# Kernel optimization log

Hardware: AMD Instinct MI355X
Metric: run time of the kernel (lower is better)

Reference implementation:

```python
import jax, jax.numpy as jnp
import numpy as np

B, S, D, H, F, M = 2, 2048, 1024, 16, 4096, 1024
HD = D // H
LR, MOM_DECAY, WD, THRESH = 0.01, 0.9, 0.01, 0.1


def rmsnorm(x, w, eps=1e-8):
    n = jnp.linalg.norm(x, axis=-1, keepdims=True) * (x.shape[-1] ** -0.5)
    return w * x / (n + eps)


def rope_sin_cos(seq_len, dim):
    inv_freq = 1.0 / (10000.0 ** (jnp.arange(0, dim, 2, dtype=jnp.float32) / dim))
    ang = jnp.arange(seq_len, dtype=jnp.float32)[:, None] * inv_freq[None, :]  # [S, dim/2]
    return jnp.sin(ang), jnp.cos(ang)


def apply_rope(x, sin, cos):
    # x: [B,H,S,hd]; sin/cos: [S,hd/2] broadcast. Matches torch source:
    # split even/odd lanes, then CONCATENATE halves (not interleave).
    x1, x2 = x[..., ::2], x[..., 1::2]
    return jnp.concatenate([x1 * cos - x2 * sin, x1 * sin + x2 * cos], axis=-1)


def lmm_mlp(z, w0, b0, w1, b1):
    return jnp.maximum(z @ w0 + b0, 0.0) @ w1 + b1


def setup_inputs() -> dict:
    key = jax.random.key(0)
    k = jax.random.split(key, 20)
    sc = 0.02
    r = lambda i, shape: jax.random.normal(k[i], shape, jnp.float32) * sc
    return {
        'x': jax.random.normal(k[0], (B, S, D), jnp.float32),
        'mask': jnp.tril(jnp.ones((1, 1, S, S), dtype=bool)),
        'wq': r(1, (D, D)), 'wk': r(2, (D, D)), 'wv': r(3, (D, D)), 'wo': r(4, (D, D)),
        'n1': jnp.ones(D, jnp.float32), 'n2': jnp.ones(D, jnp.float32), 'n3': jnp.ones(D, jnp.float32),
        'ffn_w1': r(5, (D, F)), 'ffn_w2': r(6, (D, F)), 'ffn_w3': r(7, (F, D)),
        'pk_w': r(8, (D, M)), 'pk_b': jnp.zeros(M, jnp.float32),
        'pv_w': r(9, (D, M)), 'pv_b': jnp.zeros(M, jnp.float32),
        'pq_w': r(10, (D, M)), 'pq_b': jnp.zeros(M, jnp.float32),
        'l0_w': r(11, (M, M)), 'l0_b': jnp.zeros(M, jnp.float32),
        'l1_w': r(12, (M, M)), 'l1_b': jnp.zeros(M, jnp.float32),
        'm0_w': jnp.zeros((M, M), jnp.float32), 'm0_b': jnp.zeros(M, jnp.float32),
        'm1_w': jnp.zeros((M, M), jnp.float32), 'm1_b': jnp.zeros(M, jnp.float32),
    }


def reference(x, mask, wq, wk, wv, wo, n1, n2, n3, ffn_w1, ffn_w2, ffn_w3,
              pk_w, pk_b, pv_w, pv_b, pq_w, pq_b,
              l0_w, l0_b, l1_w, l1_b, m0_w, m0_b, m1_w, m1_b):
    # ---- attention sublayer (pre-norm, RoPE) ----
    hn = rmsnorm(x, n1)
    q = (hn @ wq).reshape(B, S, H, HD).transpose(0, 2, 1, 3)
    kk = (hn @ wk).reshape(B, S, H, HD).transpose(0, 2, 1, 3)
    v = (hn @ wv).reshape(B, S, H, HD).transpose(0, 2, 1, 3)
    sin, cos = rope_sin_cos(S, HD)
    q = apply_rope(q, sin, cos)
    kk = apply_rope(kk, sin, cos)
    scores = jnp.einsum('bhqd,bhkd->bhqk', q, kk) / np.sqrt(HD).astype(np.float32)
    scores = jnp.where(mask, scores, -jnp.inf)
    attn = jax.nn.softmax(scores, axis=-1)
    o = jnp.einsum('bhqk,bhkd->bhqd', attn, v).transpose(0, 2, 1, 3).reshape(B, S, D)
    h = x + o @ wo

    # ---- neural memory sublayer ----
    hn2 = rmsnorm(h, n2)
    q_lmm = hn2 @ pq_w + pq_b
    retrieved = lmm_mlp(q_lmm, l0_w, l0_b, l1_w, l1_b)  # uses PRE-update params

    # online Titan-style LMM update (torch does this under no_grad, after retrieval)
    kf = jax.lax.stop_gradient((hn2 @ pk_w + pk_b).reshape(B * S, M))
    vf = jax.lax.stop_gradient((hn2 @ pv_w + pv_b).reshape(B * S, M))

    def lmm_loss(params):
        pred = lmm_mlp(kf, *params)
        return jnp.sum(jnp.mean((pred - vf) ** 2, axis=-1))

    params = (l0_w, l0_b, l1_w, l1_b)
    loss_sum, grads = jax.value_and_grad(lmm_loss)(params)
    avg_loss = loss_sum / (B * S)
    do_update = avg_loss >= THRESH
    moms = (m0_w, m0_b, m1_w, m1_b)
    new_moms, new_params = [], []
    for p, m, g in zip(params, moms, grads):
        nm = MOM_DECAY * m - LR * g
        np_ = p * (1.0 - WD) + nm
        new_moms.append(jnp.where(do_update, nm, m))
        new_params.append(jnp.where(do_update, np_, p))

    h = h + retrieved

    # ---- SwiGLU FFN sublayer ----
    hn3 = rmsnorm(h, n3)
    ffn = (jax.nn.silu(hn3 @ ffn_w1) * (hn3 @ ffn_w2)) @ ffn_w3
    out = h + ffn
    return (out, *new_params, *new_moms)
```

## Files before the change

kernel.cpp:

```cpp
#include <hip/hip_runtime.h>
#include <cstdint>
#include <cstddef>

typedef __bf16 bf16;
typedef __bf16 bf16x2 __attribute__((ext_vector_type(2)));
typedef __bf16 bf16x4 __attribute__((ext_vector_type(4)));
typedef __bf16 bf16x8 __attribute__((ext_vector_type(8)));
typedef float  f32x4  __attribute__((ext_vector_type(4)));
typedef __attribute__((address_space(1))) unsigned int u32_g;
typedef __attribute__((address_space(3))) unsigned int u32_l;

#define DI __device__ __forceinline__

constexpr int Bc = 2, Sc = 2048, Dc = 1024, Hc = 16, HDc = 64, Fc = 4096, Mc = 1024;
constexpr int NTc = Bc * Sc;

DI void llds16(const bf16* g, bf16* l) {
  __builtin_amdgcn_global_load_lds((const u32_g*)g, (u32_l*)l, 16, 0, 0);
}
DI f32x4 cvt4(bf16x4 a) {
  f32x4 r; r[0] = (float)a[0]; r[1] = (float)a[1]; r[2] = (float)a[2]; r[3] = (float)a[3];
  return r;
}

__global__ void k_detect(const unsigned short* __restrict__ x, int* __restrict__ flag)
{
  const int tid = threadIdx.x;
  int cnt = 0;
#pragma unroll
  for (int i = 0; i < 8; i++) {
    unsigned short h = x[tid * 8 + i];
    int e = (h >> 7) & 0xFF;
    if (e < 96 || e > 160) cnt++;
  }
#pragma unroll
  for (int off = 32; off > 0; off >>= 1) cnt += __shfl_down(cnt, off, 64);
  if (tid == 0) *flag = (cnt > 32) ? 1 : 0;
}

__global__ __launch_bounds__(256)
void k_cvt(const void* __restrict__ src, bf16* __restrict__ dst, int n4, const int* __restrict__ flag)
{
  int i = blockIdx.x * 256 + threadIdx.x;
  if (i >= n4) return;
  bf16x4 o;
  if (*flag) {
    f32x4 v = ((const f32x4*)src)[i];
    o[0] = (bf16)v[0]; o[1] = (bf16)v[1]; o[2] = (bf16)v[2]; o[3] = (bf16)v[3];
  } else {
    o = ((const bf16x4*)src)[i];
  }
  ((bf16x4*)dst)[i] = o;
}

__global__ void k_transpose_dt(const void* __restrict__ src, bf16* __restrict__ dst,
                               int R, int C, const int* __restrict__ flag)
{
  __shared__ bf16 tile[32][33];
  const int c0 = blockIdx.x * 32, r0 = blockIdx.y * 32;
  const int tx = threadIdx.x, ty = threadIdx.y;
  const bool f32 = (*flag != 0);
  for (int i = ty; i < 32; i += 8) {
    size_t idx = (size_t)(r0 + i) * C + (c0 + tx);
    tile[i][tx] = f32 ? (bf16)((const float*)src)[idx] : ((const bf16*)src)[idx];
  }
  __syncthreads();
  for (int i = ty; i < 32; i += 8)
    dst[(size_t)(c0 + i) * R + (r0 + tx)] = tile[tx][i];
}

__global__ void k_transpose_v(const bf16* __restrict__ v, bf16* __restrict__ vt)
{
  __shared__ bf16 tile[32][33];
  const int d0 = blockIdx.x * 32, s0 = blockIdx.y * 32;
  const int bh = blockIdx.z;
  const int b = bh >> 4, hh = bh & 15;
  const int tx = threadIdx.x, ty = threadIdx.y;
  for (int i = ty; i < 32; i += 8)
    tile[i][tx] = v[((size_t)(b * Sc + s0 + i)) * Dc + hh * HDc + d0 + tx];
  __syncthreads();
  for (int i = ty; i < 32; i += 8)
    vt[((size_t)(bh * HDc + d0 + i)) * Sc + s0 + tx] = tile[tx][i];
}

enum EpiMode { EPI_BF16 = 0, EPI_BIAS_BF16, EPI_BIAS_RELU_BF16, EPI_BIAS_RESB_F32,
               EPI_SILU_BF16, EPI_DZ_BF16, EPI_RESX_BF16, EPI_RESF_F32,
               EPI_SEGC_BF16, EPI_SEGC_BIAS_BF16, EPI_SEG2_RELU_BF16, EPI_ATOMIC_F32 };

template <int EPI>
__global__ __launch_bounds__(256)
void k_gemm(const bf16* __restrict__ A, const bf16* __restrict__ Bt,
            int Mr, int Nr, int Kr,
            float* outF, bf16* outB,
            const bf16* __restrict__ bias, const bf16* auxB,
            const float* resF,
            const void* __restrict__ resX, const int* __restrict__ flag)
{
  __shared__ bf16 As[128 * 32];
  __shared__ bf16 Bs[128 * 32];
  const int tid = threadIdx.x;
  const int w = tid >> 6, l = tid & 63;
  const int wr = w >> 1, wc = w & 1;
  const int row0 = blockIdx.y * 128, col0 = blockIdx.x * 128;

  const f32x4 vzero = {0.f, 0.f, 0.f, 0.f};
  f32x4 acc[4][4];
#pragma unroll
  for (int i = 0; i < 4; i++)
#pragma unroll
    for (int j = 0; j < 4; j++) acc[i][j] = vzero;

  const bf16* Ag = A + (size_t)(row0 + w * 16 + (l >> 2)) * Kr + ((l & 3) << 3);
  const bf16* Bg = Bt + (size_t)(col0 + w * 16 + (l >> 2)) * Kr + ((l & 3) << 3);
  bf16* AsW = &As[w * 512];
  bf16* BsW = &Bs[w * 512];
  const size_t rowHop = (size_t)64 * Kr;

  const int chunk = Kr / gridDim.z;
  const int kbeg = blockIdx.z * chunk;

  for (int k0 = kbeg; k0 < kbeg + chunk; k0 += 32) {
    __syncthreads();
    llds16(Ag + k0, AsW);
    llds16(Ag + rowHop + k0, AsW + 2048);
    llds16(Bg + k0, BsW);
    llds16(Bg + rowHop + k0, BsW + 2048);
    __syncthreads();
    bf16x8 af[4], bfr[4];
#pragma unroll
    for (int mt = 0; mt < 4; mt++)
      af[mt] = *(const bf16x8*)&As[(wr * 64 + mt * 16 + (l & 15)) * 32 + (l >> 4) * 8];
#pragma unroll
    for (int nt = 0; nt < 4; nt++)
      bfr[nt] = *(const bf16x8*)&Bs[(wc * 64 + nt * 16 + (l & 15)) * 32 + (l >> 4) * 8];
#pragma unroll
    for (int mt = 0; mt < 4; mt++)
#pragma unroll
      for (int nt = 0; nt < 4; nt++)
        acc[mt][nt] = __builtin_amdgcn_mfma_f32_16x16x32_bf16(af[mt], bfr[nt], acc[mt][nt], 0, 0, 0);
  }

  const bool f32res = (EPI == EPI_RESX_BF16) ? (*flag != 0) : false;
  float biasv[4];
  if (EPI == EPI_BIAS_BF16 || EPI == EPI_BIAS_RELU_BF16 || EPI == EPI_BIAS_RESB_F32 ||
      EPI == EPI_SEGC_BIAS_BF16 || EPI == EPI_SEG2_RELU_BF16) {
#pragma unroll
    for (int nt = 0; nt < 4; nt++)
      biasv[nt] = (float)bias[col0 + wc * 64 + nt * 16 + (l & 15)];
  }
#pragma unroll
  for (int mt = 0; mt < 4; mt++) {
    const int rowb = row0 + wr * 64 + mt * 16 + ((l >> 4) << 2);
    float av[4][4];
    if (EPI == EPI_SILU_BF16 || EPI == EPI_DZ_BF16 || EPI == EPI_BIAS_RESB_F32) {
#pragma unroll
      for (int nt = 0; nt < 4; nt++) {
        const int col = col0 + wc * 64 + nt * 16 + (l & 15);
#pragma unroll
        for (int r = 0; r < 4; r++)
          av[nt][r] = (float)auxB[(size_t)(rowb + r) * Nr + col];
      }
    }
    if (EPI == EPI_RESF_F32) {
#pragma unroll
      for (int nt = 0; nt < 4; nt++) {
        const int col = col0 + wc * 64 + nt * 16 + (l & 15);
#pragma unroll
        for (int r = 0; r < 4; r++)
          av[nt][r] = resF[(size_t)(rowb + r) * Nr + col];
      }
    }
    if (EPI == EPI_RESX_BF16) {
#pragma unroll
      for (int nt = 0; nt < 4; nt++) {
        const int col = col0 + wc * 64 + nt * 16 + (l & 15);
#pragma unroll
        for (int r = 0; r < 4; r++) {
          const size_t idx = (size_t)(rowb + r) * Nr + col;
          av[nt][r] = f32res ? ((const float*)resX)[idx] : (float)((const bf16*)resX)[idx];
        }
      }
    }
#pragma unroll
    for (int nt = 0; nt < 4; nt++) {
      const int col = col0 + wc * 64 + nt * 16 + (l & 15);
#pragma unroll
      for (int r = 0; r < 4; r++) {
        const size_t idx = (size_t)(rowb + r) * Nr + col;
        float v = acc[mt][nt][r];
        if (EPI == EPI_BF16) { outB[idx] = (bf16)v; }
        else if (EPI == EPI_BIAS_BF16) { outB[idx] = (bf16)(v + biasv[nt]); }
        else if (EPI == EPI_BIAS_RELU_BF16) { outB[idx] = (bf16)fmaxf(v + biasv[nt], 0.f); }
        else if (EPI == EPI_BIAS_RESB_F32) { outF[idx] = v + biasv[nt] + av[nt][r]; }
        else if (EPI == EPI_SILU_BF16) {
          float s1v = av[nt][r];
          float sl = s1v / (1.f + __expf(-s1v));
          outB[idx] = (bf16)(sl * v);
        }
        else if (EPI == EPI_DZ_BF16) { outB[idx] = (bf16)(av[nt][r] > 0.f ? v : 0.f); }
        else if (EPI == EPI_RESX_BF16) { outB[idx] = (bf16)(v + av[nt][r]); }
        else if (EPI == EPI_RESF_F32) { outF[idx] = v + av[nt][r]; }
        else if (EPI == EPI_SEGC_BF16 || EPI == EPI_SEGC_BIAS_BF16) {
          const size_t sidx = (size_t)(col >> 10) * ((size_t)NTc * 1024)
                            + (size_t)(rowb + r) * 1024 + (col & 1023);
          float vv = (EPI == EPI_SEGC_BIAS_BF16) ? (v + biasv[nt]) : v;
          outB[sidx] = (bf16)vv;
        }
        else if (EPI == EPI_SEG2_RELU_BF16) {
          bf16* ob = (rowb >> 12) ? (bf16*)outF : outB;
          ob[(size_t)((rowb + r) & 4095) * 1024 + col] = (bf16)fmaxf(v + biasv[nt], 0.f);
        }
        else if (EPI == EPI_ATOMIC_F32) {
          atomicAdd(&outF[(size_t)(rowb + r) * Nr + col], v);
        }
      }
    }
  }
}

__global__ __launch_bounds__(256)
void k_gemm_tn(const bf16* __restrict__ X, const bf16* __restrict__ Y, int Kt,
               float* __restrict__ out)
{
  __shared__ bf16 As[128 * 36];
  __shared__ bf16 Bs[128 * 36];
  const int tid = threadIdx.x;
  const int w = tid >> 6, l = tid & 63;
  const int wr = w >> 1, wc = w & 1;
  const int row0 = blockIdx.y * 128, col0 = blockIdx.x * 128;
  const int iofs = (tid & 15) * 8;
  const int tp   = (tid >> 4) * 2;

  const f32x4 vzero = {0.f, 0.f, 0.f, 0.f};
  f32x4 acc[4][4];
#pragma unroll
  for (int i = 0; i < 4; i++)
#pragma unroll
    for (int j = 0; j < 4; j++) acc[i][j] = vzero;

  const int chunk = Kt / gridDim.z;
  const int tbeg = blockIdx.z * chunk;

  for (int t0 = tbeg; t0 < tbeg + chunk; t0 += 32) {
    __syncthreads();
    bf16x8 a0 = *(const bf16x8*)&X[(size_t)(t0 + tp) * 1024 + row0 + iofs];
    bf16x8 a1 = *(const bf16x8*)&X[(size_t)(t0 + tp + 1) * 1024 + row0 + iofs];
    bf16x8 b0 = *(const bf16x8*)&Y[(size_t)(t0 + tp) * 1024 + col0 + iofs];
    bf16x8 b1 = *(const bf16x8*)&Y[(size_t)(t0 + tp + 1) * 1024 + col0 + iofs];
#pragma unroll
    for (int e = 0; e < 8; e++) {
      bf16x2 pa; pa[0] = a0[e]; pa[1] = a1[e];
      bf16x2 pb; pb[0] = b0[e]; pb[1] = b1[e];
      *(bf16x2*)&As[(iofs + e) * 36 + tp] = pa;
      *(bf16x2*)&Bs[(iofs + e) * 36 + tp] = pb;
    }
    __syncthreads();
    bf16x8 af[4], bfr[4];
#pragma unroll
    for (int mt = 0; mt < 4; mt++) {
      const int base = (wr * 64 + mt * 16 + (l & 15)) * 36 + (l >> 4) * 8;
      bf16x4 lo = *(const bf16x4*)&As[base];
      bf16x4 hi = *(const bf16x4*)&As[base + 4];
#pragma unroll
      for (int e = 0; e < 4; e++) { af[mt][e] = lo[e]; af[mt][4 + e] = hi[e]; }
    }
#pragma unroll
    for (int nt = 0; nt < 4; nt++) {
      const int base = (wc * 64 + nt * 16 + (l & 15)) * 36 + (l >> 4) * 8;
      bf16x4 lo = *(const bf16x4*)&Bs[base];
      bf16x4 hi = *(const bf16x4*)&Bs[base + 4];
#pragma unroll
      for (int e = 0; e < 4; e++) { bfr[nt][e] = lo[e]; bfr[nt][4 + e] = hi[e]; }
    }
#pragma unroll
    for (int mt = 0; mt < 4; mt++)
#pragma unroll
      for (int nt = 0; nt < 4; nt++)
        acc[mt][nt] = __builtin_amdgcn_mfma_f32_16x16x32_bf16(af[mt], bfr[nt], acc[mt][nt], 0, 0, 0);
  }

#pragma unroll
  for (int mt = 0; mt < 4; mt++) {
    const int rowb = row0 + wr * 64 + mt * 16 + ((l >> 4) << 2);
#pragma unroll
    for (int nt = 0; nt < 4; nt++) {
      const int col = col0 + wc * 64 + nt * 16 + (l & 15);
#pragma unroll
      for (int r = 0; r < 4; r++)
        atomicAdd(&out[(size_t)(rowb + r) * 1024 + col], acc[mt][nt][r]);
    }
  }
}

__global__ __launch_bounds__(256)
void k_rmsnorm_dt(const void* __restrict__ x, const bf16* __restrict__ w, bf16* __restrict__ out,
                  const int* __restrict__ flag)
{
  const int row = blockIdx.x;
  const int tid = threadIdx.x;
  f32x4 xv;
  if (*flag) xv = *(const f32x4*)((const float*)x + (size_t)row * Dc + tid * 4);
  else       xv = cvt4(*(const bf16x4*)((const bf16*)x + (size_t)row * Dc + tid * 4));
  float ss = xv[0] * xv[0] + xv[1] * xv[1] + xv[2] * xv[2] + xv[3] * xv[3];
#pragma unroll
  for (int off = 32; off > 0; off >>= 1) ss += __shfl_down(ss, off, 64);
  __shared__ float part[4];
  if ((tid & 63) == 0) part[tid >> 6] = ss;
  __syncthreads();
  float tot = part[0] + part[1] + part[2] + part[3];
  float inv = 1.f / (sqrtf(tot) * 0.03125f + 1e-8f);
  bf16x4 wb = *(const bf16x4*)(w + tid * 4);
  bf16x4 ov;
  ov[0] = (bf16)((float)wb[0] * xv[0] * inv);
  ov[1] = (bf16)((float)wb[1] * xv[1] * inv);
  ov[2] = (bf16)((float)wb[2] * xv[2] * inv);
  ov[3] = (bf16)((float)wb[3] * xv[3] * inv);
  *(bf16x4*)(out + (size_t)row * Dc + tid * 4) = ov;
}

__global__ __launch_bounds__(256)
void k_rmsnorm_b(const bf16* __restrict__ x, const bf16* __restrict__ w, bf16* __restrict__ out)
{
  const int row = blockIdx.x;
  const int tid = threadIdx.x;
  f32x4 xv = cvt4(*(const bf16x4*)(x + (size_t)row * Dc + tid * 4));
  float ss = xv[0] * xv[0] + xv[1] * xv[1] + xv[2] * xv[2] + xv[3] * xv[3];
#pragma unroll
  for (int off = 32; off > 0; off >>= 1) ss += __shfl_down(ss, off, 64);
  __shared__ float part[4];
  if ((tid & 63) == 0) part[tid >> 6] = ss;
  __syncthreads();
  float tot = part[0] + part[1] + part[2] + part[3];
  float inv = 1.f / (sqrtf(tot) * 0.03125f + 1e-8f);
  bf16x4 wb = *(const bf16x4*)(w + tid * 4);
  bf16x4 ov;
  ov[0] = (bf16)((float)wb[0] * xv[0] * inv);
  ov[1] = (bf16)((float)wb[1] * xv[1] * inv);
  ov[2] = (bf16)((float)wb[2] * xv[2] * inv);
  ov[3] = (bf16)((float)wb[3] * xv[3] * inv);
  *(bf16x4*)(out + (size_t)row * Dc + tid * 4) = ov;
}

__global__ __launch_bounds__(256)
void k_rmsnorm_f(const float* __restrict__ x, const bf16* __restrict__ w, bf16* __restrict__ out)
{
  const int row = blockIdx.x;
  const int tid = threadIdx.x;
  f32x4 xv = *(const f32x4*)(x + (size_t)row * Dc + tid * 4);
  float ss = xv[0] * xv[0] + xv[1] * xv[1] + xv[2] * xv[2] + xv[3] * xv[3];
#pragma unroll
  for (int off = 32; off > 0; off >>= 1) ss += __shfl_down(ss, off, 64);
  __shared__ float part[4];
  if ((tid & 63) == 0) part[tid >> 6] = ss;
  __syncthreads();
  float tot = part[0] + part[1] + part[2] + part[3];
  float inv = 1.f / (sqrtf(tot) * 0.03125f + 1e-8f);
  bf16x4 wb = *(const bf16x4*)(w + tid * 4);
  bf16x4 ov;
  ov[0] = (bf16)((float)wb[0] * xv[0] * inv);
  ov[1] = (bf16)((float)wb[1] * xv[1] * inv);
  ov[2] = (bf16)((float)wb[2] * xv[2] * inv);
  ov[3] = (bf16)((float)wb[3] * xv[3] * inv);
  *(bf16x4*)(out + (size_t)row * Dc + tid * 4) = ov;
}

__global__ __launch_bounds__(256)
void k_rope(bf16* __restrict__ q, bf16* __restrict__ kx)
{
  const int idx = blockIdx.x * 256 + threadIdx.x;
  const int t = idx >> 4, hh = idx & 15;
  const int s = t & (Sc - 1);
  float sn[32], cs[32];
#pragma unroll
  for (int i = 0; i < 32; i++) {
    float f = expf(-(float)i * 0.28782313662425574f);
    float ang = (float)s * f;
    sn[i] = sinf(ang);
    cs[i] = cosf(ang);
  }
  for (int pass = 0; pass < 2; pass++) {
    bf16* p = (pass ? kx : q) + (size_t)t * Dc + hh * HDc;
    float xb[64], ob[64];
#pragma unroll
    for (int j = 0; j < 16; j++) *(f32x4*)&xb[j * 4] = cvt4(*(const bf16x4*)(p + j * 4));
#pragma unroll
    for (int i = 0; i < 32; i++) {
      float x1 = xb[2 * i], x2 = xb[2 * i + 1];
      ob[i] = x1 * cs[i] - x2 * sn[i];
      ob[32 + i] = x1 * sn[i] + x2 * cs[i];
    }
#pragma unroll
    for (int j = 0; j < 16; j++) {
      bf16x4 o4;
      o4[0] = (bf16)ob[j * 4]; o4[1] = (bf16)ob[j * 4 + 1];
      o4[2] = (bf16)ob[j * 4 + 2]; o4[3] = (bf16)ob[j * 4 + 3];
      *(bf16x4*)(p + j * 4) = o4;
    }
  }
}

__global__ __launch_bounds__(256)
void k_attn(const bf16* __restrict__ q, const bf16* __restrict__ kx,
            const bf16* __restrict__ vt, bf16* __restrict__ o)
{
  constexpr int PAD = 72;
  __shared__ __align__(16) char smem[19456];

  const int blk = blockIdx.x;
  const int qi = 127 - (blk >> 5);
  const int bh = blk & 31;
  const int b = bh >> 4, hh = bh & 15;
  const int tid = threadIdx.x;
  const int w = tid >> 6, l = tid & 63;
  const int quad = l >> 4, c = l & 15;

  bf16* Psw = (bf16*)smem + w * 16 * PAD;
  float* Buf = (float*)smem;

  const int qrow = qi * 16 + c;
  const size_t qbase = ((size_t)(b * Sc + qrow)) * Dc + hh * HDc;
  bf16x8 qf0 = *(const bf16x8*)(q + qbase + quad * 8);
  bf16x8 qf1 = *(const bf16x8*)(q + qbase + 32 + quad * 8);
#pragma unroll
  for (int j = 0; j < 8; j++) {
    qf0[j] = (bf16)((float)qf0[j] * 0.125f);
    qf1[j] = (bf16)((float)qf1[j] * 0.125f);
  }

  const f32x4 vzero = {0.f, 0.f, 0.f, 0.f};
  f32x4 oacc[4];
#pragma unroll
  for (int nt = 0; nt < 4; nt++) oacc[nt] = vzero;
  float mrun[4] = {-3.0e38f, -3.0e38f, -3.0e38f, -3.0e38f};
  float lrun[4] = {0.f, 0.f, 0.f, 0.f};

  const int qrow0 = qi * 16 + quad * 4;
  const int ntiles = (qi >> 2) + 1;

  const bf16* kb = kx + (size_t)b * Sc * Dc + hh * HDc;
  const bf16* vb = vt + (size_t)bh * HDc * Sc;

  for (int t0 = w; t0 < ntiles; t0 += 4) {
    const int kk0 = t0 * 64;

    f32x4 sf[4];
#pragma unroll
    for (int nt = 0; nt < 4; nt++) {
      const bf16* kr = kb + (size_t)(kk0 + nt * 16 + c) * Dc + quad * 8;
      bf16x8 k0 = *(const bf16x8*)kr;
      bf16x8 k1 = *(const bf16x8*)(kr + 32);
      f32x4 a = vzero;
      a = __builtin_amdgcn_mfma_f32_16x16x32_bf16(qf0, k0, a, 0, 0, 0);
      a = __builtin_amdgcn_mfma_f32_16x16x32_bf16(qf1, k1, a, 0, 0, 0);
      sf[nt] = a;
    }
    if (t0 == ntiles - 1) {
#pragma unroll
      for (int nt = 0; nt < 4; nt++)
#pragma unroll
        for (int r = 0; r < 4; r++)
          if (kk0 + nt * 16 + c > qrow0 + r) sf[nt][r] = -3.0e38f;
    }

    float mnew[4], alpha[4];
#pragma unroll
    for (int r = 0; r < 4; r++) {
      float mt = fmaxf(fmaxf(sf[0][r], sf[1][r]), fmaxf(sf[2][r], sf[3][r]));
      mt = fmaxf(mt, __shfl_xor(mt, 1, 64));
      mt = fmaxf(mt, __shfl_xor(mt, 2, 64));
      mt = fmaxf(mt, __shfl_xor(mt, 4, 64));
      mt = fmaxf(mt, __shfl_xor(mt, 8, 64));
      mnew[r] = fmaxf(mrun[r], mt);
      alpha[r] = __expf(mrun[r] - mnew[r]);
      mrun[r] = mnew[r];
    }
    float ps[4] = {0.f, 0.f, 0.f, 0.f};
#pragma unroll
    for (int nt = 0; nt < 4; nt++)
#pragma unroll
      for (int r = 0; r < 4; r++) {
        float p = __expf(sf[nt][r] - mnew[r]);
        sf[nt][r] = p;
        ps[r] += p;
      }
#pragma unroll
    for (int r = 0; r < 4; r++) {
      ps[r] += __shfl_xor(ps[r], 1, 64);
      ps[r] += __shfl_xor(ps[r], 2, 64);
      ps[r] += __shfl_xor(ps[r], 4, 64);
      ps[r] += __shfl_xor(ps[r], 8, 64);
      lrun[r] = lrun[r] * alpha[r] + ps[r];
    }
#pragma unroll
    for (int nt = 0; nt < 4; nt++)
#pragma unroll
      for (int r = 0; r < 4; r++) oacc[nt][r] *= alpha[r];

#pragma unroll
    for (int nt = 0; nt < 4; nt++)
#pragma unroll
      for (int r = 0; r < 4; r++)
        Psw[(quad * 4 + r) * PAD + nt * 16 + c] = (bf16)sf[nt][r];
    bf16x8 pa0 = *(const bf16x8*)&Psw[c * PAD + quad * 8];
    bf16x8 pa1 = *(const bf16x8*)&Psw[c * PAD + 32 + quad * 8];

#pragma unroll
    for (int nt = 0; nt < 4; nt++) {
      const bf16* vr = vb + (size_t)(nt * 16 + c) * Sc + kk0 + quad * 8;
      bf16x8 v0 = *(const bf16x8*)vr;
      bf16x8 v1 = *(const bf16x8*)(vr + 32);
      oacc[nt] = __builtin_amdgcn_mfma_f32_16x16x32_bf16(pa0, v0, oacc[nt], 0, 0, 0);
      oacc[nt] = __builtin_amdgcn_mfma_f32_16x16x32_bf16(pa1, v1, oacc[nt], 0, 0, 0);
    }
  }

  __syncthreads();
  if (w > 0) {
    float* dst = Buf + ((w - 1) * 64 + l) * 25;
#pragma unroll
    for (int nt = 0; nt < 4; nt++)
#pragma unroll
      for (int r = 0; r < 4; r++) dst[nt * 4 + r] = oacc[nt][r];
#pragma unroll
    for (int r = 0; r < 4; r++) { dst[16 + r] = mrun[r]; dst[20 + r] = lrun[r]; }
  }
  __syncthreads();
  if (w == 0) {
#pragma unroll
    for (int w2 = 0; w2 < 3; w2++) {
      const float* src = Buf + (w2 * 64 + l) * 25;
      float m2[4], l2[4];
#pragma unroll
      for (int r = 0; r < 4; r++) { m2[r] = src[16 + r]; l2[r] = src[20 + r]; }
#pragma unroll
      for (int r = 0; r < 4; r++) {
        float mn = fmaxf(mrun[r], m2[r]);
        float a = __expf(mrun[r] - mn);
        float bb = __expf(m2[r] - mn);
        lrun[r] = lrun[r] * a + l2[r] * bb;
        mrun[r] = mn;
#pragma unroll
        for (int nt = 0; nt < 4; nt++)
          oacc[nt][r] = oacc[nt][r] * a + src[nt * 4 + r] * bb;
      }
    }
    float inv[4];
#pragma unroll
    for (int r = 0; r < 4; r++) inv[r] = 1.f / lrun[r];
#pragma unroll
    for (int r = 0; r < 4; r++) {
      const size_t obase = ((size_t)(b * Sc + qrow0 + r)) * Dc + hh * HDc;
#pragma unroll
      for (int nt = 0; nt < 4; nt++)
        o[obase + nt * 16 + c] = (bf16)(oacc[nt][r] * inv[r]);
    }
  }
}

__global__ __launch_bounds__(256)
void k_dpred(bf16* __restrict__ predDp, const bf16* __restrict__ vf, float* __restrict__ loss)
{
  __shared__ float red[4];
  const int tid = threadIdx.x;
  const size_t n8 = (size_t)NTc * Mc / 8;
  float lacc = 0.f;
  for (size_t i = (size_t)blockIdx.x * 256 + tid; i < n8; i += (size_t)gridDim.x * 256) {
    bf16x8 p8 = ((const bf16x8*)predDp)[i];
    bf16x8 v8 = ((const bf16x8*)vf)[i];
    bf16x8 d8;
#pragma unroll
    for (int e = 0; e < 8; e++) {
      float df = (float)p8[e] - (float)v8[e];
      lacc += df * df;
      d8[e] = (bf16)(df * (2.0f / 1024.0f));
    }
    ((bf16x8*)predDp)[i] = d8;
  }
#pragma unroll
  for (int off = 32; off > 0; off >>= 1) lacc += __shfl_down(lacc, off, 64);
  if ((tid & 63) == 0) red[tid >> 6] = lacc;
  __syncthreads();
  if (tid == 0) atomicAdd(loss, red[0] + red[1] + red[2] + red[3]);
}

__global__ __launch_bounds__(256)
void k_colsum(const bf16* __restrict__ X, float* __restrict__ out, int C, int rowsPer)
{
  int c = blockIdx.x * 256 + threadIdx.x;
  int r0 = blockIdx.y * rowsPer;
  float s = 0.f;
#pragma unroll 8
  for (int r = r0; r < r0 + rowsPer; r++) s += (float)X[(size_t)r * C + c];
  atomicAdd(&out[c], s);
}

__global__ __launch_bounds__(256)
void k_update_dt(const void* __restrict__ p0w, const void* __restrict__ p0b,
                 const void* __restrict__ p1w, const void* __restrict__ p1b,
                 const void* __restrict__ m0w, const void* __restrict__ m0b,
                 const void* __restrict__ m1w, const void* __restrict__ m1b,
                 const float* __restrict__ g0wF, const float* __restrict__ g0b,
                 const float* __restrict__ g1wF, const float* __restrict__ g1b,
                 const float* __restrict__ loss, const int* __restrict__ flag,
                 float* __restrict__ outP, float* __restrict__ outM)
{
  const int i = blockIdx.x * 256 + threadIdx.x;
  const bool upd = (loss[0] >= 0.1f * 1024.f * 4096.f);
  const bool f32 = (*flag != 0);
  constexpr int W = 1024 * 1024;
  const void *pp, *pm; int j; float g;
  if (i < W) { pp = p0w; pm = m0w; j = i; g = g0wF[i]; }
  else if (i < W + 1024) { j = i - W; pp = p0b; pm = m0b; g = g0b[j]; }
  else if (i < 2 * W + 1024) { j = i - W - 1024; pp = p1w; pm = m1w; g = g1wF[j]; }
  else { j = i - 2 * W - 1024; pp = p1b; pm = m1b; g = g1b[j]; }
  float p = f32 ? ((const float*)pp)[j] : (float)((const bf16*)pp)[j];
  float m = f32 ? ((const float*)pm)[j] : (float)((const bf16*)pm)[j];
  float nm = 0.9f * m - 0.01f * g;
  float np = 0.99f * p + nm;
  outP[i] = upd ? np : p;
  outM[i] = upd ? nm : m;
}

extern "C" void kernel_launch(void* const* d_in, const int* in_sizes, int n_in,
                              void* d_out, int out_size, void* d_ws, size_t ws_size,
                              hipStream_t stream)
{
  (void)in_sizes; (void)n_in; (void)out_size; (void)ws_size;
  const void* x   = d_in[0];
  const void* wq  = d_in[2];
  const void* wk  = d_in[3];
  const void* wv  = d_in[4];
  const void* wo  = d_in[5];
  const void* n1  = d_in[6];
  const void* n2  = d_in[7];
  const void* n3  = d_in[8];
  const void* fw1 = d_in[9];
  const void* fw2 = d_in[10];
  const void* fw3 = d_in[11];
  const void* pkw = d_in[12];
  const void* pkb = d_in[13];
  const void* pvw = d_in[14];
  const void* pvb = d_in[15];
  const void* pqw = d_in[16];
  const void* pqb = d_in[17];
  const void* l0w = d_in[18];
  const void* l0b = d_in[19];
  const void* l1w = d_in[20];
  const void* l1b = d_in[21];
  const void* m0w = d_in[22];
  const void* m0b = d_in[23];
  const void* m1w = d_in[24];
  const void* m1b = d_in[25];

  char* ws = (char*)d_ws;
  size_t off = 0;
  auto alloc = [&](size_t bytes) -> char* {
    char* p = ws + off;
    off += (bytes + 255) & ~(size_t)255;
    return p;
  };

  const size_t DD = (size_t)Dc * Dc;
  const size_t ND = (size_t)NTc * Dc;
  const size_t MB8 = 2 * ND;
  const size_t M1 = DD;

  bf16* W = (bf16*)alloc(2 * 8 * M1);
  bf16 *wqT = W, *wkT = W + M1, *wvT = W + 2 * M1, *woT = W + 3 * M1;
  bf16 *pqT = W + 4 * M1, *pkT = W + 5 * M1, *pvT = W + 6 * M1, *l0T = W + 7 * M1;
  bf16 *l1T = W + M1;
  bf16 *h1buf = W + 2 * M1;
  bf16 *l1c = W;
  bf16 *w1T = W + 4 * M1;
  bf16 *w2T = W;
  bf16 *w3T = W + 4 * M1;

  bf16* B0 = (bf16*)alloc(MB8);
  bf16* B1 = (bf16*)alloc(MB8);
  bf16* B2 = (bf16*)alloc(MB8);
  bf16* B3 = (bf16*)alloc(MB8);
  bf16* B4 = (bf16*)alloc(MB8);
  bf16* s1 = B0;
  bf16* VtG = B4;

  float* g0b = (float*)alloc(4 * 1024);
  float* g1b = (float*)alloc(4 * 1024);
  float* lossb = (float*)alloc(256);
  int*   flag  = (int*)alloc(256);
  bf16* n1c = (bf16*)alloc(2 * 1024);
  bf16* n2c = (bf16*)alloc(2 * 1024);
  bf16* n3c = (bf16*)alloc(2 * 1024);
  bf16* bqkv = (bf16*)alloc(2 * 3072);
  bf16* b0c = (bf16*)alloc(2 * 1024);
  bf16* b1c = (bf16*)alloc(2 * 1024);

  float* outX = (float*)d_out;
  float* outP = outX + ND;
  float* outM = outP + (2 * DD + 2048);
  float* g0wF = outM;
  float* g1wF = outM + M1 + 1024;
  bf16*  hn   = (bf16*)outX;

  const dim3 tb(32, 8);

  hipMemsetAsync(lossb, 0, sizeof(float), stream);
  hipMemsetAsync(g0b, 0, 4 * 1024, stream);
  hipMemsetAsync(g1b, 0, 4 * 1024, stream);
  hipMemsetAsync(outM, 0, (2 * M1 + 2048) * sizeof(float), stream);
  k_detect<<<1, 64, 0, stream>>>((const unsigned short*)x, flag);

  k_cvt<<<1, 256, 0, stream>>>(n1, n1c, 256, flag);
  k_cvt<<<1, 256, 0, stream>>>(n2, n2c, 256, flag);
  k_cvt<<<1, 256, 0, stream>>>(n3, n3c, 256, flag);
  k_cvt<<<1, 256, 0, stream>>>(pqb, bqkv, 256, flag);
  k_cvt<<<1, 256, 0, stream>>>(pkb, bqkv + 1024, 256, flag);
  k_cvt<<<1, 256, 0, stream>>>(pvb, bqkv + 2048, 256, flag);
  k_cvt<<<1, 256, 0, stream>>>(l0b, b0c, 256, flag);
  k_cvt<<<1, 256, 0, stream>>>(l1b, b1c, 256, flag);

  k_transpose_dt<<<dim3(32, 32), tb, 0, stream>>>(wq, wqT, Dc, Dc, flag);
  k_transpose_dt<<<dim3(32, 32), tb, 0, stream>>>(wk, wkT, Dc, Dc, flag);
  k_transpose_dt<<<dim3(32, 32), tb, 0, stream>>>(wv, wvT, Dc, Dc, flag);
  k_transpose_dt<<<dim3(32, 32), tb, 0, stream>>>(wo, woT, Dc, Dc, flag);
  k_transpose_dt<<<dim3(32, 32), tb, 0, stream>>>(pqw, pqT, Dc, Mc, flag);
  k_transpose_dt<<<dim3(32, 32), tb, 0, stream>>>(pkw, pkT, Dc, Mc, flag);
  k_transpose_dt<<<dim3(32, 32), tb, 0, stream>>>(pvw, pvT, Dc, Mc, flag);
  k_transpose_dt<<<dim3(32, 32), tb, 0, stream>>>(l0w, l0T, Mc, Mc, flag);

  k_rmsnorm_dt<<<NTc, 256, 0, stream>>>(x, n1c, hn, flag);
  k_gemm<EPI_SEGC_BF16><<<dim3(24, 32), 256, 0, stream>>>(hn, wqT, NTc, 3072, Dc, nullptr, B0, nullptr, nullptr, nullptr, nullptr, nullptr);
  k_transpose_v<<<dim3(2, 64, 32), tb, 0, stream>>>(B2, VtG);
  k_rope<<<256, 256, 0, stream>>>(B0, B1);
  k_attn<<<4096, 256, 0, stream>>>(B0, B1, VtG, B3);
  k_gemm<EPI_RESX_BF16><<<dim3(8, 32), 256, 0, stream>>>(B3, woT, NTc, Dc, Dc, nullptr, B4, nullptr, nullptr, nullptr, x, flag);
  k_transpose_dt<<<dim3(32, 32), tb, 0, stream>>>(l1w, l1T, Mc, Mc, flag);

  k_rmsnorm_b<<<NTc, 256, 0, stream>>>(B4, n2c, B0);
  k_gemm<EPI_SEGC_BIAS_BF16><<<dim3(24, 32), 256, 0, stream>>>(B0, pqT, NTc, 3072, Dc, nullptr, B1, bqkv, nullptr, nullptr, nullptr, nullptr);
  k_gemm<EPI_SEG2_RELU_BF16><<<dim3(8, 64), 256, 0, stream>>>(B1, l0T, 2 * NTc, Mc, Mc, (float*)h1buf, B0, b0c, nullptr, nullptr, nullptr, nullptr);
  k_gemm<EPI_BIAS_RESB_F32><<<dim3(8, 32), 256, 0, stream>>>(B0, l1T, NTc, Mc, Mc, outX, nullptr, b1c, B4, nullptr, nullptr, nullptr);
  k_gemm<EPI_BIAS_BF16><<<dim3(8, 32), 256, 0, stream>>>(h1buf, l1T, NTc, Mc, Mc, nullptr, B1, b1c, nullptr, nullptr, nullptr, nullptr);

  k_cvt<<<1024, 256, 0, stream>>>(l1w, l1c, (int)(DD / 4), flag);
  k_dpred<<<256, 256, 0, stream>>>(B1, B3, lossb);
  k_gemm<EPI_DZ_BF16><<<dim3(8, 32), 256, 0, stream>>>(B1, l1c, NTc, Mc, Mc, nullptr, B3, nullptr, h1buf, nullptr, nullptr, nullptr);
  k_gemm_tn<<<dim3(8, 8, 8), 256, 0, stream>>>(h1buf, B1, NTc, g1wF);
  k_gemm_tn<<<dim3(8, 8, 8), 256, 0, stream>>>(B2, B3, NTc, g0wF);
  k_transpose_dt<<<dim3(128, 32), tb, 0, stream>>>(fw1, w1T, Dc, Fc, flag);
  k_colsum<<<dim3(4, 32), 256, 0, stream>>>(B1, g1b, Mc, NTc / 32);
  k_colsum<<<dim3(4, 32), 256, 0, stream>>>(B3, g0b, Mc, NTc / 32);
  k_update_dt<<<8200, 256, 0, stream>>>(l0w, l0b, l1w, l1b, m0w, m0b, m1w, m1b,
                                        g0wF, g0b, g1wF, g1b, lossb, flag, outP, outM);

  k_transpose_dt<<<dim3(128, 32), tb, 0, stream>>>(fw2, w2T, Dc, Fc, flag);
  k_rmsnorm_f<<<NTc, 256, 0, stream>>>(outX, n3c, B4);
  k_gemm<EPI_BF16><<<dim3(32, 32), 256, 0, stream>>>(B4, w1T, NTc, Fc, Dc, nullptr, s1, nullptr, nullptr, nullptr, nullptr, nullptr);
  k_transpose_dt<<<dim3(32, 128), tb, 0, stream>>>(fw3, w3T, Fc, Dc, flag);
  k_gemm<EPI_SILU_BF16><<<dim3(32, 32), 256, 0, stream>>>(B4, w2T, NTc, Fc, Dc, nullptr, s1, nullptr, s1, nullptr, nullptr, nullptr);
  k_gemm<EPI_ATOMIC_F32><<<dim3(8, 32, 2), 256, 0, stream>>>(s1, w3T, NTc, Dc, Fc, outX, nullptr, nullptr, nullptr, nullptr, nullptr, nullptr);
}
```

Baseline: 980.7 us.

## Rewrite causal attention with 32x32 MFMA and per-wave query tiles

The attention kernel now gives each wave its own 32-row query tile and uses 32x32x16 bf16 MFMA, computing S transposed so the softmax row statistics stay within a lane pair. P is rearranged into the next MFMA's operand layout through cross-half lane shuffles instead of an LDS round trip. This removes the shared-memory cross-wave merge and the barriers, and cuts the grid from 4096 to 512 blocks. The cost is fewer blocks, so occupancy and load balance are lower, and the causal work per wave is uneven across the four waves of a block.

```diff
diff --git a/kernel.cpp b/kernel.cpp
--- a/kernel.cpp
+++ b/kernel.cpp
@@ -7,6 +7,7 @@
 typedef __bf16 bf16x4 __attribute__((ext_vector_type(4)));
 typedef __bf16 bf16x8 __attribute__((ext_vector_type(8)));
 typedef float  f32x4  __attribute__((ext_vector_type(4)));
+typedef float  f32x16 __attribute__((ext_vector_type(16)));
 typedef __attribute__((address_space(1))) unsigned int u32_g;
 typedef __attribute__((address_space(3))) unsigned int u32_l;
 
@@ -403,157 +404,112 @@
 void k_attn(const bf16* __restrict__ q, const bf16* __restrict__ kx,
             const bf16* __restrict__ vt, bf16* __restrict__ o)
 {
-  constexpr int PAD = 72;
-  __shared__ __align__(16) char smem[19456];
+  union UV { bf16x8 v; unsigned int u[4]; };
+  union UH { bf16x2 h; unsigned int u; };
 
   const int blk = blockIdx.x;
-  const int qi = 127 - (blk >> 5);
+  const int g  = 15 - (blk >> 5);
   const int bh = blk & 31;
   const int b = bh >> 4, hh = bh & 15;
   const int tid = threadIdx.x;
   const int w = tid >> 6, l = tid & 63;
-  const int quad = l >> 4, c = l & 15;
-
-  bf16* Psw = (bf16*)smem + w * 16 * PAD;
-  float* Buf = (float*)smem;
-
-  const int qrow = qi * 16 + c;
-  const size_t qbase = ((size_t)(b * Sc + qrow)) * Dc + hh * HDc;
-  bf16x8 qf0 = *(const bf16x8*)(q + qbase + quad * 8);
-  bf16x8 qf1 = *(const bf16x8*)(q + qbase + 32 + quad * 8);
-#pragma unroll
-  for (int j = 0; j < 8; j++) {
-    qf0[j] = (bf16)((float)qf0[j] * 0.125f);
-    qf1[j] = (bf16)((float)qf1[j] * 0.125f);
-  }
-
-  const f32x4 vzero = {0.f, 0.f, 0.f, 0.f};
-  f32x4 oacc[4];
-#pragma unroll
-  for (int nt = 0; nt < 4; nt++) oacc[nt] = vzero;
-  float mrun[4] = {-3.0e38f, -3.0e38f, -3.0e38f, -3.0e38f};
-  float lrun[4] = {0.f, 0.f, 0.f, 0.f};
-
-  const int qrow0 = qi * 16 + quad * 4;
-  const int ntiles = (qi >> 2) + 1;
+  const int hi = l >> 5, lq = l & 31;
+
+  const int q0 = g * 128 + w * 32;
+  const int ntiles = g * 4 + w + 1;
 
   const bf16* kb = kx + (size_t)b * Sc * Dc + hh * HDc;
   const bf16* vb = vt + (size_t)bh * HDc * Sc;
 
-  for (int t0 = w; t0 < ntiles; t0 += 4) {
-    const int kk0 = t0 * 64;
-
-    f32x4 sf[4];
-#pragma unroll
-    for (int nt = 0; nt < 4; nt++) {
-      const bf16* kr = kb + (size_t)(kk0 + nt * 16 + c) * Dc + quad * 8;
-      bf16x8 k0 = *(const bf16x8*)kr;
-      bf16x8 k1 = *(const bf16x8*)(kr + 32);
-      f32x4 a = vzero;
-      a = __builtin_amdgcn_mfma_f32_16x16x32_bf16(qf0, k0, a, 0, 0, 0);
-      a = __builtin_amdgcn_mfma_f32_16x16x32_bf16(qf1, k1, a, 0, 0, 0);
-      sf[nt] = a;
-    }
+  bf16x8 qf[4];
+  {
+    const bf16* qp = q + ((size_t)(b * Sc + q0 + lq)) * Dc + hh * HDc + hi * 8;
+#pragma unroll
+    for (int ds = 0; ds < 4; ds++) {
+      qf[ds] = *(const bf16x8*)(qp + ds * 16);
+#pragma unroll
+      for (int j = 0; j < 8; j++) qf[ds][j] = (bf16)((float)qf[ds][j] * 0.125f);
+    }
+  }
+
+  f32x16 oacc0, oacc1;
+#pragma unroll
+  for (int j = 0; j < 16; j++) { oacc0[j] = 0.f; oacc1[j] = 0.f; }
+  float mrun = -3.0e38f, lrun = 0.f;
+
+  for (int t0 = 0; t0 < ntiles; t0++) {
+    const int kk0 = t0 * 32;
+
+    const bf16* kp = kb + (size_t)(kk0 + lq) * Dc + hi * 8;
+    f32x16 sacc;
+#pragma unroll
+    for (int j = 0; j < 16; j++) sacc[j] = 0.f;
+#pragma unroll
+    for (int ds = 0; ds < 4; ds++) {
+      bf16x8 kf = *(const bf16x8*)(kp + ds * 16);
+      sacc = __builtin_amdgcn_mfma_f32_32x32x16_bf16(kf, qf[ds], sacc, 0, 0, 0);
+    }
+
     if (t0 == ntiles - 1) {
 #pragma unroll
-      for (int nt = 0; nt < 4; nt++)
-#pragma unroll
-        for (int r = 0; r < 4; r++)
-          if (kk0 + nt * 16 + c > qrow0 + r) sf[nt][r] = -3.0e38f;
-    }
-
-    float mnew[4], alpha[4];
-#pragma unroll
-    for (int r = 0; r < 4; r++) {
-      float mt = fmaxf(fmaxf(sf[0][r], sf[1][r]), fmaxf(sf[2][r], sf[3][r]));
-      mt = fmaxf(mt, __shfl_xor(mt, 1, 64));
-      mt = fmaxf(mt, __shfl_xor(mt, 2, 64));
-      mt = fmaxf(mt, __shfl_xor(mt, 4, 64));
-      mt = fmaxf(mt, __shfl_xor(mt, 8, 64));
-      mnew[r] = fmaxf(mrun[r], mt);
-      alpha[r] = __expf(mrun[r] - mnew[r]);
-      mrun[r] = mnew[r];
-    }
-    float ps[4] = {0.f, 0.f, 0.f, 0.f};
-#pragma unroll
-    for (int nt = 0; nt < 4; nt++)
-#pragma unroll
-      for (int r = 0; r < 4; r++) {
-        float p = __expf(sf[nt][r] - mnew[r]);
-        sf[nt][r] = p;
-        ps[r] += p;
+      for (int reg = 0; reg < 16; reg++) {
+        const int kidx = (reg & 3) + 8 * (reg >> 2) + 4 * hi;
+        sacc[reg] = (kidx > lq) ? -3.0e38f : sacc[reg];
       }
-#pragma unroll
-    for (int r = 0; r < 4; r++) {
-      ps[r] += __shfl_xor(ps[r], 1, 64);
-      ps[r] += __shfl_xor(ps[r], 2, 64);
-      ps[r] += __shfl_xor(ps[r], 4, 64);
-      ps[r] += __shfl_xor(ps[r], 8, 64);
-      lrun[r] = lrun[r] * alpha[r] + ps[r];
-    }
-#pragma unroll
-    for (int nt = 0; nt < 4; nt++)
-#pragma unroll
-      for (int r = 0; r < 4; r++) oacc[nt][r] *= alpha[r];
-
-#pragma unroll
-    for (int nt = 0; nt < 4; nt++)
-#pragma unroll
-      for (int r = 0; r < 4; r++)
-        Psw[(quad * 4 + r) * PAD + nt * 16 + c] = (bf16)sf[nt][r];
-    bf16x8 pa0 = *(const bf16x8*)&Psw[c * PAD + quad * 8];
-    bf16x8 pa1 = *(const bf16x8*)&Psw[c * PAD + 32 + quad * 8];
-
-#pragma unroll
-    for (int nt = 0; nt < 4; nt++) {
-      const bf16* vr = vb + (size_t)(nt * 16 + c) * Sc + kk0 + quad * 8;
-      bf16x8 v0 = *(const bf16x8*)vr;
-      bf16x8 v1 = *(const bf16x8*)(vr + 32);
-      oacc[nt] = __builtin_amdgcn_mfma_f32_16x16x32_bf16(pa0, v0, oacc[nt], 0, 0, 0);
-      oacc[nt] = __builtin_amdgcn_mfma_f32_16x16x32_bf16(pa1, v1, oacc[nt], 0, 0, 0);
-    }
-  }
-
-  __syncthreads();
-  if (w > 0) {
-    float* dst = Buf + ((w - 1) * 64 + l) * 25;
-#pragma unroll
-    for (int nt = 0; nt < 4; nt++)
-#pragma unroll
-      for (int r = 0; r < 4; r++) dst[nt * 4 + r] = oacc[nt][r];
-#pragma unroll
-    for (int r = 0; r < 4; r++) { dst[16 + r] = mrun[r]; dst[20 + r] = lrun[r]; }
-  }
-  __syncthreads();
-  if (w == 0) {
-#pragma unroll
-    for (int w2 = 0; w2 < 3; w2++) {
-      const float* src = Buf + (w2 * 64 + l) * 25;
-      float m2[4], l2[4];
-#pragma unroll
-      for (int r = 0; r < 4; r++) { m2[r] = src[16 + r]; l2[r] = src[20 + r]; }
-#pragma unroll
-      for (int r = 0; r < 4; r++) {
-        float mn = fmaxf(mrun[r], m2[r]);
-        float a = __expf(mrun[r] - mn);
-        float bb = __expf(m2[r] - mn);
-        lrun[r] = lrun[r] * a + l2[r] * bb;
-        mrun[r] = mn;
-#pragma unroll
-        for (int nt = 0; nt < 4; nt++)
-          oacc[nt][r] = oacc[nt][r] * a + src[nt * 4 + r] * bb;
-      }
-    }
-    float inv[4];
-#pragma unroll
-    for (int r = 0; r < 4; r++) inv[r] = 1.f / lrun[r];
-#pragma unroll
-    for (int r = 0; r < 4; r++) {
-      const size_t obase = ((size_t)(b * Sc + qrow0 + r)) * Dc + hh * HDc;
-#pragma unroll
-      for (int nt = 0; nt < 4; nt++)
-        o[obase + nt * 16 + c] = (bf16)(oacc[nt][r] * inv[r]);
-    }
+    }
+
+    float mx = sacc[0];
+#pragma unroll
+    for (int reg = 1; reg < 16; reg++) mx = fmaxf(mx, sacc[reg]);
+    mx = fmaxf(mx, __shfl_xor(mx, 32, 64));
+
+    const float mnew = fmaxf(mrun, mx);
+    const float al = __expf(mrun - mnew);
+    mrun = mnew;
+    float p[16], ps = 0.f;
+#pragma unroll
+    for (int reg = 0; reg < 16; reg++) { p[reg] = __expf(sacc[reg] - mnew); ps += p[reg]; }
+    ps += __shfl_xor(ps, 32, 64);
+    lrun = lrun * al + ps;
+#pragma unroll
+    for (int j = 0; j < 16; j++) { oacc0[j] *= al; oacc1[j] *= al; }
+
+    unsigned int wv[8];
+#pragma unroll
+    for (int m = 0; m < 8; m++) {
+      UH t; t.h[0] = (bf16)p[2 * m]; t.h[1] = (bf16)p[2 * m + 1];
+      wv[m] = t.u;
+    }
+    const unsigned int ex0 = __shfl_xor(hi ? wv[0] : wv[2], 32, 64);
+    const unsigned int ex1 = __shfl_xor(hi ? wv[1] : wv[3], 32, 64);
+    const unsigned int ex2 = __shfl_xor(hi ? wv[4] : wv[6], 32, 64);
+    const unsigned int ex3 = __shfl_xor(hi ? wv[5] : wv[7], 32, 64);
+    UV pa0, pa1;
+    pa0.u[0] = hi ? ex0 : wv[0];  pa0.u[1] = hi ? ex1 : wv[1];
+    pa0.u[2] = hi ? wv[2] : ex0;  pa0.u[3] = hi ? wv[3] : ex1;
+    pa1.u[0] = hi ? ex2 : wv[4];  pa1.u[1] = hi ? ex3 : wv[5];
+    pa1.u[2] = hi ? wv[6] : ex2;  pa1.u[3] = hi ? wv[7] : ex3;
+
+    const bf16* vp = vb + (size_t)lq * Sc + kk0 + hi * 8;
+    bf16x8 v00 = *(const bf16x8*)(vp);
+    bf16x8 v10 = *(const bf16x8*)(vp + 16);
+    bf16x8 v01 = *(const bf16x8*)(vp + (size_t)32 * Sc);
+    bf16x8 v11 = *(const bf16x8*)(vp + (size_t)32 * Sc + 16);
+    oacc0 = __builtin_amdgcn_mfma_f32_32x32x16_bf16(v00, pa0.v, oacc0, 0, 0, 0);
+    oacc0 = __builtin_amdgcn_mfma_f32_32x32x16_bf16(v10, pa1.v, oacc0, 0, 0, 0);
+    oacc1 = __builtin_amdgcn_mfma_f32_32x32x16_bf16(v01, pa0.v, oacc1, 0, 0, 0);
+    oacc1 = __builtin_amdgcn_mfma_f32_32x32x16_bf16(v11, pa1.v, oacc1, 0, 0, 0);
+  }
+
+  const float inv = 1.f / lrun;
+  bf16* op = o + ((size_t)(b * Sc + q0 + lq)) * Dc + hh * HDc;
+#pragma unroll
+  for (int m = 0; m < 8; m++) {
+    const int d0 = (2 * m & 3) + 8 * (m >> 1) + 4 * hi;
+    UH t0v; t0v.h[0] = (bf16)(oacc0[2 * m] * inv); t0v.h[1] = (bf16)(oacc0[2 * m + 1] * inv);
+    *(unsigned int*)(op + d0) = t0v.u;
+    UH t1v; t1v.h[0] = (bf16)(oacc1[2 * m] * inv); t1v.h[1] = (bf16)(oacc1[2 * m + 1] * inv);
+    *(unsigned int*)(op + 32 + d0) = t1v.u;
   }
 }
 
@@ -731,7 +687,7 @@
   k_gemm<EPI_SEGC_BF16><<<dim3(24, 32), 256, 0, stream>>>(hn, wqT, NTc, 3072, Dc, nullptr, B0, nullptr, nullptr, nullptr, nullptr, nullptr);
   k_transpose_v<<<dim3(2, 64, 32), tb, 0, stream>>>(B2, VtG);
   k_rope<<<256, 256, 0, stream>>>(B0, B1);
-  k_attn<<<4096, 256, 0, stream>>>(B0, B1, VtG, B3);
+  k_attn<<<512, 256, 0, stream>>>(B0, B1, VtG, B3);
   k_gemm<EPI_RESX_BF16><<<dim3(8, 32), 256, 0, stream>>>(B3, woT, NTc, Dc, Dc, nullptr, B4, nullptr, nullptr, nullptr, x, flag);
   k_transpose_dt<<<dim3(32, 32), tb, 0, stream>>>(l1w, l1T, Mc, Mc, flag);
 
```

New measurement: 954.1 us. 2.7% less time.
